# Kernel tuning notes

Hardware: AMD Instinct MI355X
Metric: run time of the kernel (lower is better)

## Reference

```python
import jax, jax.numpy as jnp
import numpy as np
from jax import lax

KS = 10      # kernel_size (asserted == 10 in the torch module)
DCT_N = 10   # dct_n


def _dct_pair(N):
    k = np.arange(N)[:, None]
    i = np.arange(N)[None, :]
    w = np.full((N, 1), np.sqrt(2.0 / N))
    w[0, 0] = np.sqrt(1.0 / N)
    d = w * np.cos(np.pi * (i + 0.5) * k / N)
    return jnp.asarray(d, jnp.float32), jnp.asarray(np.linalg.inv(d), jnp.float32)


def _conv1d(x, w):
    # x: [B, C, L], w: [O, C, K], VALID conv (bias=False in torch)
    return lax.conv_general_dilated(x, w, (1,), 'VALID',
                                    dimension_numbers=('NCH', 'OIH', 'NCH'))


def _two_conv(x, w1, w2):
    return jax.nn.relu(_conv1d(jax.nn.relu(_conv1d(x, w1)), w2))


def _gconv(x, w, att, b):
    # GraphConvolution: att @ (x @ w) + b ; x: [B, node, f_in]
    return jnp.einsum('nm,bmo->bno', att, jnp.einsum('bmf,fo->bmo', x, w)) + b


def _gcn(x, gc1_w, gc1_att, gc1_b, gcb_w, gcb_att, gcb_b, gc7_w, gc7_att, gc7_b):
    # Standard motion-prediction GCN (eval mode: BN=identity, dropout off)
    y = jnp.tanh(_gconv(x, gc1_w, gc1_att, gc1_b))
    for s in range(gcb_w.shape[0]):  # small fixed num_stage
        h = jnp.tanh(_gconv(y, gcb_w[s, 0], gcb_att[s, 0], gcb_b[s, 0]))
        h = jnp.tanh(_gconv(h, gcb_w[s, 1], gcb_att[s, 1], gcb_b[s, 1]))
        y = y + h
    return _gconv(y, gc7_w, gc7_att, gc7_b) + x


def _ffc(x, wl, wg):
    # RealFFC(dim=3): spectral branch (rFFT over time, 1x1 conv on real/imag,
    # ReLU, irFFT) + local 1x1 branch. x: [B, 3, F/3, T]
    y = jnp.fft.rfft(x, axis=-1)
    yc = jnp.concatenate([y.real, y.imag], axis=1)            # [B, 6, F/3, K]
    yc = jax.nn.relu(jnp.einsum('oc,bcfk->bofk', wg, yc))
    re, im = jnp.split(yc, 2, axis=1)
    spec = jnp.fft.irfft(re + 1j * im, n=x.shape[-1], axis=-1)
    return jnp.einsum('oc,bcft->boft', wl, x) + spec


def _forward(input_seq, wq1, wq2, wk1, wk2,
             gc1_w, gc1_att, gc1_b, gcb_w, gcb_att, gcb_b,
             gc7_w, gc7_att, gc7_b, mlp_w1, mlp_w2, ffc_wl, ffc_wg,
             output_n, input_n):
    seq = input_seq[:, :input_n]
    B, _, F = seq.shape
    blen = KS + output_n                       # DCT block length (30)
    dctm, idctm = _dct_pair(blen)
    key_seq = jnp.swapaxes(seq, 1, 2)[:, :, :input_n - output_n]
    query_seq = jnp.swapaxes(seq, 1, 2)[:, :, -KS:]
    # im2col-style overlapping temporal blocks -> per-block DCT
    nvb = input_n - blen + 1
    idx = np.arange(blen)[None, :] + np.arange(nvb)[:, None]
    blocks = seq[:, idx]                       # [B, nvb, blen, F]
    # matches torch reshape(...,dct_n,-1).transpose(2,3).reshape: feature-major
    dvb = jnp.einsum('dk,bnkf->bnfd', dctm[:DCT_N], blocks).reshape(B, nvb, -1)
    key_feat = _two_conv(key_seq / 1000.0, wk1, wk2)       # [B, D, nvb]
    query_feat = _two_conv(query_seq / 1000.0, wq1, wq2)   # [B, D, 1]
    score = jnp.einsum('bdq,bdk->bqk', query_feat, key_feat) + 1e-15
    attn = score / jnp.sum(score, axis=2, keepdims=True)   # sum-normalized attention
    attended = jnp.einsum('bqk,bkf->bqf', attn, dvb)[:, 0].reshape(B, F, DCT_N)
    # FFC branch: pad with last frame x10, fold F into (3, F//3)
    ffc_in = jnp.concatenate([seq, jnp.repeat(seq[:, -1:], 10, axis=1)], axis=1)
    ffc_in = jnp.swapaxes(ffc_in, 1, 2).reshape(B, 3, F // 3, input_n + 10)
    ffc_out = _ffc(ffc_in, ffc_wl, ffc_wg).reshape(B, F, input_n + 10)[:, :, :DCT_N]
    ffc_out = jnp.swapaxes(ffc_out, 1, 2)      # [B, DCT_N, F]
    # GCN branch: last KS frames + last frame repeated output_n times
    gidx = np.concatenate([np.arange(input_n - KS, input_n),
                           np.full(output_n, input_n - 1)])
    gcn_in = seq[:, gidx]                      # [B, blen, F]
    dct_in = jnp.einsum('dk,bkf->bfd', dctm[:DCT_N], gcn_in)
    gcn_out = _gcn(dct_in, gc1_w, gc1_att, gc1_b, gcb_w, gcb_att, gcb_b,
                   gc7_w, gc7_att, gc7_b)      # [B, F, DCT_N]
    combined = jnp.concatenate([gcn_out, attended], axis=-1)
    recon = jnp.einsum('kd,bfd->bkf', idctm[:, :DCT_N], combined[:, :, :DCT_N])  # [B, blen, F]
    fused = jnp.swapaxes(jnp.concatenate([recon, ffc_out], axis=1), 1, 2)  # [B, F, blen+DCT_N=40]
    h = jax.nn.relu(jnp.einsum('bft,ot->bfo', fused, mlp_w1))  # Linear(40,256), no bias
    out = jnp.einsum('bfo,to->bft', h, mlp_w2)                 # Linear(256,40), no bias
    out = jnp.swapaxes(out, 1, 2)[:, :DCT_N]   # [B, DCT_N, F]
    return out[:, :, None, :]                  # [B, DCT_N, itera=1, F]


def setup_inputs() -> dict:
    key = jax.random.key(0)
    ks = jax.random.split(key, 20)
    B, T, F, D, NS = 1024, 50, 48, 512, 2
    p = lambda k, shp: jax.random.normal(k, shp, dtype=jnp.float32) * 0.05
    return {
        'input_seq': jax.random.normal(ks[0], (B, T, F), dtype=jnp.float32),
        'wq1': p(ks[1], (D, F, 6)), 'wq2': p(ks[2], (D, D, 5)),
        'wk1': p(ks[3], (D, F, 6)), 'wk2': p(ks[4], (D, D, 5)),
        'gc1_w': p(ks[5], (10, D)), 'gc1_att': p(ks[6], (F, F)), 'gc1_b': p(ks[7], (D,)),
        'gcb_w': p(ks[8], (NS, 2, D, D)), 'gcb_att': p(ks[9], (NS, 2, F, F)),
        'gcb_b': p(ks[10], (NS, 2, D)),
        'gc7_w': p(ks[11], (D, 10)), 'gc7_att': p(ks[12], (F, F)), 'gc7_b': p(ks[13], (10,)),
        'mlp_w1': p(ks[14], (256, 40)), 'mlp_w2': p(ks[15], (40, 256)),
        'ffc_wl': p(ks[16], (3, 3)), 'ffc_wg': p(ks[17], (6, 6)),
        'output_n': 20, 'input_n': 50, 'itera': 1,
    }


def reference(input_seq, wq1, wq2, wk1, wk2, gc1_w, gc1_att, gc1_b,
              gcb_w, gcb_att, gcb_b, gc7_w, gc7_att, gc7_b,
              mlp_w1, mlp_w2, ffc_wl, ffc_wg, output_n, input_n, itera):
    assert itera == 1  # single-iteration path (the torch itera>1 branch is skipped)
    return _forward(input_seq, wq1, wq2, wk1, wk2,
                    gc1_w, gc1_att, gc1_b, gcb_w, gcb_att, gcb_b,
                    gc7_w, gc7_att, gc7_b, mlp_w1, mlp_w2, ffc_wl, ffc_wg,
                    output_n, input_n)
```

## Files before the change

### kernel.cpp

```cpp
#include <hip/hip_runtime.h>
#include <math.h>

#define BB 1024
#define TT 50
#define FF 48
#define EXTN 60
#define NFREQ 31

typedef _Float16 h8 __attribute__((ext_vector_type(8)));
typedef _Float16 h4 __attribute__((ext_vector_type(4)));
typedef float f4 __attribute__((ext_vector_type(4)));

__device__ __forceinline__ float fast_tanh(float x) {
    float e = __expf(2.0f * x);
    return 1.0f - 2.0f * __builtin_amdgcn_rcpf(e + 1.0f);
}

__global__ void prep_kernel(const float* __restrict__ gcb_w, _Float16* __restrict__ P,
                            const float* __restrict__ gc1_w, _Float16* __restrict__ P1,
                            const float* __restrict__ gc7_w, _Float16* __restrict__ P7,
                            const float* __restrict__ mlp_w1, _Float16* __restrict__ Pw1,
                            const float* __restrict__ mlp_w2, _Float16* __restrict__ Pw2,
                            const float* __restrict__ gc1_att, const float* __restrict__ gcb_att,
                            const float* __restrict__ gc7_att, _Float16* __restrict__ attp,
                            _Float16* __restrict__ Pc_hi, _Float16* __restrict__ Pc_lo,
                            _Float16* __restrict__ Pi_hi, _Float16* __restrict__ Pi_lo,
                            float* __restrict__ dctm, float* __restrict__ dtail) {
    int blk = blockIdx.x, tid = threadIdx.x;
    const _Float16 HZ = (_Float16)0.0f;
    if (blk < 512) {
        int z = blk >> 7;
        int idx = ((blk & 127) << 8) | tid;
        int lane = idx & 63, t8 = idx >> 6;
        int nt = t8 & 7, kw = t8 >> 3;
        int ks = kw & 15, wv = kw >> 4;
        int n = wv * 128 + nt * 16 + (lane & 15);
        int k0 = ks * 32 + (lane >> 4) * 8;
        const float* src = gcb_w + (size_t)z * 262144 + n;
        h8 v;
        #pragma unroll
        for (int j = 0; j < 8; ++j) v[j] = (_Float16)src[(size_t)(k0 + j) * 512];
        *(h8*)(P + (size_t)z * 262144 + (size_t)idx * 8) = v;
    } else if (blk < 528) {
        int idx = ((blk - 512) << 8) | tid;
        int lane = idx & 63, t8 = idx >> 6;
        int nt = t8 & 7, kw = t8 >> 3;
        int ks = kw & 1, wv = kw >> 1;
        int n = wv * 128 + nt * 16 + (lane & 15);
        int k0 = ks * 32 + (lane >> 4) * 8;
        h8 v;
        #pragma unroll
        for (int j = 0; j < 8; ++j) v[j] = (k0 + j < 10) ? (_Float16)gc1_w[(k0 + j) * 512 + n] : HZ;
        *(h8*)(P1 + (size_t)idx * 8) = v;
    } else if (blk < 532) {
        int idx = ((blk - 528) << 8) | tid;
        int lane = idx & 63, t8 = idx >> 6;
        int ks = t8 & 3, wv = t8 >> 2;
        int n = lane & 15;
        int k0 = wv * 128 + ks * 32 + (lane >> 4) * 8;
        h8 v;
        #pragma unroll
        for (int j = 0; j < 8; ++j) v[j] = (n < 10) ? (_Float16)gc7_w[(k0 + j) * 10 + n] : HZ;
        *(h8*)(P7 + (size_t)idx * 8) = v;
    } else if (blk < 540) {
        int idx = ((blk - 532) << 8) | tid;
        int lane = idx & 63, t8 = idx >> 6;
        int ks = t8 & 1, q = t8 >> 1;
        int nt = q & 3, wv = q >> 2;
        int o = wv * 64 + nt * 16 + (lane & 15);
        int k0 = ks * 32 + (lane >> 4) * 8;
        h8 v;
        #pragma unroll
        for (int j = 0; j < 8; ++j) v[j] = (k0 + j < 40) ? (_Float16)mlp_w1[o * 40 + k0 + j] : HZ;
        *(h8*)(Pw1 + (size_t)idx * 8) = v;
    } else if (blk < 542) {
        int idx = ((blk - 540) << 8) | tid;
        int lane = idx & 63, ks = idx >> 6;
        int m = lane & 15;
        int k0 = ks * 32 + (lane >> 4) * 8;
        h8 v;
        #pragma unroll
        for (int j = 0; j < 8; ++j) v[j] = (m < 10) ? (_Float16)mlp_w2[m * 256 + k0 + j] : HZ;
        *(h8*)(Pw2 + (size_t)idx * 8) = v;
    } else if (blk < 614) {
        int idx = (blk - 542) * 256 + tid;
        if (idx < 18432) {
            int l = idx / 3072, r = (idx % 3072) / 64, m = idx & 63;
            float v = 0.f;
            if (m < 48) {
                v = (l == 0) ? gc1_att[r * 48 + m]
                  : (l <= 4) ? gcb_att[(l - 1) * 2304 + r * 48 + m]
                             : gc7_att[r * 48 + m];
            }
            attp[idx] = (_Float16)v;
        }
    } else if (blk < 646) {
        int g = (blk - 614) * 256 + tid;
        int tab = g >> 12, e = g & 4095;
        int j = e & 7, lane = (e >> 3) & 63, t8 = e >> 9;
        int ks = t8 & 1, nt = t8 >> 1;
        int n = nt * 16 + (lane & 15);
        int t = ks * 32 + (lane >> 4) * 8 + j;
        double v = 0.0;
        if (t < 60 && n < 62)
            v = (n < 31) ? cos(M_PI * (double)(n * t) / 30.0)
                         : -sin(M_PI * (double)((n - 31) * t) / 30.0);
        _Float16 hi = (_Float16)(float)v;
        if (tab == 0) Pc_hi[e] = hi;
        else          Pc_lo[e] = (_Float16)(float)(v - (double)(float)hi);
    } else if (blk < 654) {
        int g = (blk - 646) * 256 + tid;
        int tab = g >> 10, e = g & 1023;
        int j = e & 7, lane = (e >> 3) & 63, ks = e >> 9;
        int t = lane & 15;
        int kp = ks * 32 + (lane >> 4) * 8 + j;
        double v = 0.0;
        if (kp == 0) v = 1.0 / 60.0;
        else if (kp < 30) v = (2.0 / 60.0) * cos(M_PI * (double)(kp * t) / 30.0);
        else if (kp == 30) v = ((t & 1) ? -1.0 : 1.0) / 60.0;
        else if (kp >= 32 && kp < 61) v = -(2.0 / 60.0) * sin(M_PI * (double)((kp - 31) * t) / 30.0);
        _Float16 hi = (_Float16)(float)v;
        if (tab == 0) Pi_hi[e] = hi;
        else          Pi_lo[e] = (_Float16)(float)(v - (double)(float)hi);
    } else {
        int idx = (blk - 654) * 256 + tid;
        if (idx < 900) {
            int d = idx / 30, k = idx % 30;
            double w = (d == 0) ? sqrt(1.0 / 30.0) : sqrt(2.0 / 30.0);
            dctm[idx] = (float)(w * cos(M_PI * (k + 0.5) * d / 30.0));
        } else if (idx < 910) {
            int d = idx - 900;
            double w = (d == 0) ? sqrt(1.0 / 30.0) : sqrt(2.0 / 30.0);
            double s = 0.0;
            for (int k = 10; k < 30; ++k) s += w * cos(M_PI * (k + 0.5) * d / 30.0);
            dtail[d] = (float)s;
        }
    }
}

template<int KSTEPS, int MODE>
__device__ __forceinline__ void gcn_layer(char* S, char* T,
        const _Float16* __restrict__ Pw, const _Float16* __restrict__ attp,
        const float* __restrict__ bias, h4* sv,
        int lane, int wv, int l16, int quad) {
    h8 ab[3][2];
    #pragma unroll
    for (int it = 0; it < 3; ++it)
        #pragma unroll
        for (int ks = 0; ks < 2; ++ks)
            ab[it][ks] = *(const h8*)(attp + (it * 16 + l16) * 64 + ks * 32 + quad * 8);

    f4 acc[3][8];
    #pragma unroll
    for (int mt = 0; mt < 3; ++mt)
        #pragma unroll
        for (int nt = 0; nt < 8; ++nt) acc[mt][nt] = (f4)0.0f;

    const _Float16* Pb = Pw + (size_t)wv * (KSTEPS * 8 * 512) + lane * 8;
    const int xm = l16 & 7;
    __syncthreads();

    #pragma unroll 2
    for (int ks = 0; ks < KSTEPS; ++ks) {
        h8 a[3], bfr[8];
        #pragma unroll
        for (int nt = 0; nt < 8; ++nt)
            bfr[nt] = *(const h8*)(Pb + (ks * 8 + nt) * 512);
        #pragma unroll
        for (int mt = 0; mt < 3; ++mt)
            a[mt] = *(h8*)(S + (mt * 16 + l16) * 1024 + (((ks * 4 + quad) ^ xm) << 4));
        #pragma unroll
        for (int mt = 0; mt < 3; ++mt)
            #pragma unroll
            for (int nt = 0; nt < 8; ++nt)
                acc[mt][nt] = __builtin_amdgcn_mfma_f32_16x16x32_f16(a[mt], bfr[nt], acc[mt][nt], 0, 0, 0);
    }
    __syncthreads();

    #pragma unroll
    for (int mt = 0; mt < 3; ++mt) {
        h4 hv;
        #pragma unroll
        for (int j = 0; j < 4; ++j) hv[j] = (_Float16)acc[mt][0][j];
        *(h4*)(T + l16 * 144 + (mt * 16 + quad * 4) * 2) = hv;
    }
    asm volatile("s_waitcnt lgkmcnt(0)" ::: "memory");
    h8 tf0 = *(h8*)(T + l16 * 144 + quad * 16);
    h8 tf1 = *(h8*)(T + l16 * 144 + 64 + quad * 16);

    #pragma unroll
    for (int nt = 0; nt < 8; ++nt) {
        char* Tn = T + ((nt + 1) & 1) * 2304;
        if (nt < 7) {
            #pragma unroll
            for (int mt = 0; mt < 3; ++mt) {
                h4 hv;
                #pragma unroll
                for (int j = 0; j < 4; ++j) hv[j] = (_Float16)acc[mt][nt + 1][j];
                *(h4*)(Tn + l16 * 144 + (mt * 16 + quad * 4) * 2) = hv;
            }
        }
        f4 acc2[3];
        #pragma unroll
        for (int it = 0; it < 3; ++it) {
            acc2[it] = __builtin_amdgcn_mfma_f32_16x16x32_f16(tf0, ab[it][0], (f4)0.0f, 0, 0, 0);
            acc2[it] = __builtin_amdgcn_mfma_f32_16x16x32_f16(tf1, ab[it][1], acc2[it], 0, 0, 0);
        }
        if (nt < 7) {
            asm volatile("s_waitcnt lgkmcnt(0)" ::: "memory");
            tf0 = *(h8*)(Tn + l16 * 144 + quad * 16);
            tf1 = *(h8*)(Tn + l16 * 144 + 64 + quad * 16);
        }
        const int c0 = wv * 128 + nt * 16 + quad * 4;
        const f4 bv = *(const f4*)(bias + c0);
        #pragma unroll
        for (int it = 0; it < 3; ++it) {
            int f = it * 16 + l16;
            char* sp = S + f * 1024 + (((c0 >> 3) ^ (f & 7)) << 4) + ((c0 & 7) << 1);
            if (MODE == 1) sv[nt * 3 + it] = *(h4*)sp;
            h4 o;
            #pragma unroll
            for (int j = 0; j < 4; ++j) {
                float v = fast_tanh(acc2[it][j] + bv[j]);
                if (MODE == 2) v += (float)sv[nt * 3 + it][j];
                o[j] = (_Float16)v;
            }
            *(h4*)sp = o;
        }
    }
}

__launch_bounds__(256, 2)
__global__ void gcn_fused_kernel(const float* __restrict__ seq,
                                 const _Float16* __restrict__ P1,
                                 const _Float16* __restrict__ Pm,
                                 const _Float16* __restrict__ P7,
                                 const _Float16* __restrict__ attp,
                                 const float* __restrict__ gc1_b,
                                 const float* __restrict__ gcb_b,
                                 const float* __restrict__ gc7_b,
                                 const float* __restrict__ dctm,
                                 const float* __restrict__ dtail,
                                 _Float16* __restrict__ fush) {
    __shared__ __align__(16) char smem[69888];
    char* S    = smem;
    char* R    = smem + 49152;
    char* dctf = smem + 67584;
    const int tid = threadIdx.x, lane = tid & 63, wv = tid >> 6;
    const int l16 = lane & 15, quad = lane >> 4;
    const int b = blockIdx.x;
    char* T = R + wv * 4608;

    if (tid < 120) *(f4*)(R + tid * 16) = *(const f4*)(seq + (size_t)b * 2400 + 1920 + tid * 4);
    for (int v = tid; v < 310; v += 256)
        ((float*)(R + 2048))[v] = (v < 300) ? dctm[v] : dtail[v - 300];
    __syncthreads();
    for (int v = tid; v < 480; v += 256) {
        int f = v / 10, d = v % 10;
        const float* q = (const float*)R;
        const float* L = (const float*)(R + 2048);
        float a = L[300 + d] * q[9 * 48 + f];
        #pragma unroll
        for (int k = 0; k < 10; ++k) a += L[d * 30 + k] * q[k * 48 + f];
        ((float*)dctf)[f * 12 + d] = a;
    }
    __syncthreads();
    for (int v = tid; v < 384; v += 256) {
        int m = v >> 3, g = v & 7;
        h8 w = (h8)(_Float16)0.0f;
        if (g < 2) {
            #pragma unroll
            for (int j = 0; j < 8; ++j) {
                int d = g * 8 + j;
                if (d < 10) w[j] = (_Float16)((float*)dctf)[m * 12 + d];
            }
        }
        *(h8*)(S + m * 1024 + ((g ^ (m & 7)) << 4)) = w;
    }
    for (int v = tid; v < 384; v += 256) {
        int s = v % 3, rr = v / 3;
        int r = rr & 15, wb = rr >> 4;
        *(h8*)(R + wb * 2304 + r * 144 + 96 + s * 16) = (h8)(_Float16)0.0f;
    }

    h4 sv[24];
    gcn_layer<2, 0>(S, T, P1,          attp,          gc1_b,        sv, lane, wv, l16, quad);
    gcn_layer<16, 1>(S, T, Pm,          attp + 3072,  gcb_b,        sv, lane, wv, l16, quad);
    gcn_layer<16, 2>(S, T, Pm + 262144, attp + 6144,  gcb_b + 512,  sv, lane, wv, l16, quad);
    gcn_layer<16, 1>(S, T, Pm + 524288, attp + 9216,  gcb_b + 1024, sv, lane, wv, l16, quad);
    gcn_layer<16, 2>(S, T, Pm + 786432, attp + 12288, gcb_b + 1536, sv, lane, wv, l16, quad);

    __syncthreads();
    {
        f4 acc[3];
        #pragma unroll
        for (int mt = 0; mt < 3; ++mt) acc[mt] = (f4)0.0f;
        const _Float16* Pb7 = P7 + wv * 2048 + lane * 8;
        #pragma unroll
        for (int ks = 0; ks < 4; ++ks) {
            h8 bfr = *(const h8*)(Pb7 + ks * 512);
            int kh = wv * 128 + ks * 32;
            #pragma unroll
            for (int mt = 0; mt < 3; ++mt) {
                h8 a = *(h8*)(S + (mt * 16 + l16) * 1024 + ((((kh >> 3) + quad) ^ (l16 & 7)) << 4));
                acc[mt] = __builtin_amdgcn_mfma_f32_16x16x32_f16(a, bfr, acc[mt], 0, 0, 0);
            }
        }
        #pragma unroll
        for (int mt = 0; mt < 3; ++mt)
            *(f4*)(R + wv * 3072 + l16 * 192 + (mt * 16 + quad * 4) * 4) = acc[mt];
    }
    __syncthreads();
    if (wv == 0) {
        h4 tw[3]; int ns[3], ms[3];
        #pragma unroll
        for (int q = 0; q < 3; ++q) {
            int idx = lane * 3 + q;
            int n = idx / 12, m0 = (idx % 12) * 4;
            f4 s = *(f4*)(R + n * 192 + m0 * 4);
            s += *(f4*)(R + 3072 + n * 192 + m0 * 4);
            s += *(f4*)(R + 6144 + n * 192 + m0 * 4);
            s += *(f4*)(R + 9216 + n * 192 + m0 * 4);
            h4 h;
            #pragma unroll
            for (int j = 0; j < 4; ++j) h[j] = (_Float16)s[j];
            tw[q] = h; ns[q] = n; ms[q] = m0;
        }
        asm volatile("s_waitcnt lgkmcnt(0)" ::: "memory");
        #pragma unroll
        for (int q = 0; q < 3; ++q) *(h4*)(R + ns[q] * 144 + ms[q] * 2) = tw[q];
        if (lane < 48) {
            int row = lane / 3, s2 = lane % 3;
            *(h8*)(R + row * 144 + 96 + s2 * 16) = (h8)(_Float16)0.0f;
        }
        asm volatile("s_waitcnt lgkmcnt(0)" ::: "memory");
        h8 tf0 = *(h8*)(R + l16 * 144 + quad * 16);
        h8 tf1 = *(h8*)(R + l16 * 144 + 64 + quad * 16);
        const _Float16* a7 = attp + 15360;
        f4 acc2[3];
        #pragma unroll
        for (int it = 0; it < 3; ++it) {
            h8 ab0 = *(const h8*)(a7 + (it * 16 + l16) * 64 + quad * 8);
            h8 ab1 = *(const h8*)(a7 + (it * 16 + l16) * 64 + 32 + quad * 8);
            acc2[it] = __builtin_amdgcn_mfma_f32_16x16x32_f16(tf0, ab0, (f4)0.0f, 0, 0, 0);
            acc2[it] = __builtin_amdgcn_mfma_f32_16x16x32_f16(tf1, ab1, acc2[it], 0, 0, 0);
        }
        char* G = R + 4096;
        #pragma unroll
        for (int it = 0; it < 3; ++it) {
            int f = it * 16 + l16;
            #pragma unroll
            for (int j = 0; j < 4; ++j) {
                int c = quad * 4 + j;
                if (c < 10) {
                    float v = acc2[it][j] + gc7_b[c] + ((float*)dctf)[f * 12 + c];
                    *(float*)(G + f * 64 + c * 4) = v;
                }
            }
        }
    }
    __syncthreads();
    {
        char* G = R + 4096;
        _Float16* fb = fush + (size_t)b * 3456;
        for (int v = tid; v < 1440; v += 256) {
            int f = v / 30, t = v % 30;
            float s = 0.f;
            #pragma unroll
            for (int d = 0; d < 10; ++d) s += dctm[d * 30 + t] * *(float*)(G + f * 64 + d * 4);
            fb[f * 72 + t] = (_Float16)s;
        }
        for (int v = tid; v < 1152; v += 256) {
            int f = v / 24, t = 40 + v % 24;
            fb[f * 72 + t] = (_Float16)0.0f;
        }
    }
}

__launch_bounds__(256, 3)
__global__ void ffc_mlp_kernel(const float* __restrict__ seq,
                               const _Float16* __restrict__ fush,
                               const float* __restrict__ wl,
                               const float* __restrict__ wg,
                               const _Float16* __restrict__ Pw1,
                               const _Float16* __restrict__ Pw2,
                               const _Float16* __restrict__ Pc_hi,
                               const _Float16* __restrict__ Pc_lo,
                               const _Float16* __restrict__ Pi_hi,
                               const _Float16* __restrict__ Pi_lo,
                               float* __restrict__ out) {
    __shared__ __align__(16) char smem[44736];
    float* ext     = (float*)smem;
    char*  extT_hi = smem + 11520;
    char*  extT_lo = smem + 18432;
    char*  Ya_hi   = extT_hi;
    char*  Ya_lo   = extT_lo;
    float* Xre     = (float*)(smem + 25344);
    float* Xim     = (float*)(smem + 31488);
    _Float16* fus  = (_Float16*)(smem + 37632);
    float* wls     = (float*)(smem + 44544);
    float* wgs     = (float*)(smem + 44580);
    _Float16* hlds = (_Float16*)smem;
    char*  R2      = smem + 25344;

    const int b = blockIdx.x, tid = threadIdx.x;
    const int lane = tid & 63, wv = tid >> 6;
    const int l16 = lane & 15, quad = lane >> 4;
    const float* s = seq + (size_t)b * TT * FF;

    for (int idx = tid; idx < EXTN * FF; idx += 256) {
        int t = idx / FF, f = idx % FF;
        ext[idx] = s[(t < TT ? t : TT - 1) * FF + f];
    }
    for (int idx = tid; idx < 64 * FF; idx += 256) {
        int t = idx / FF, f = idx % FF;
        float v = (t < EXTN) ? s[(t < TT ? t : TT - 1) * FF + f] : 0.f;
        _Float16 hi = (_Float16)v;
        ((_Float16*)(extT_hi + f * 144))[t] = hi;
        ((_Float16*)(extT_lo + f * 144))[t] = (_Float16)(v - (float)hi);
    }
    if (tid < 9) wls[tid] = wl[tid];
    if (tid >= 64 && tid < 100) wgs[tid - 64] = wg[tid - 64];
    __syncthreads();

    {
        const int nt = wv;
        f4 acc[3];
        #pragma unroll
        for (int mt = 0; mt < 3; ++mt) acc[mt] = (f4)0.0f;
        #pragma unroll
        for (int ks = 0; ks < 2; ++ks) {
            h8 bhi = *(const h8*)(Pc_hi + (nt * 2 + ks) * 512 + lane * 8);
            h8 blo = *(const h8*)(Pc_lo + (nt * 2 + ks) * 512 + lane * 8);
            #pragma unroll
            for (int mt = 0; mt < 3; ++mt) {
                h8 ahi = *(h8*)(extT_hi + (mt * 16 + l16) * 144 + ks * 64 + quad * 16);
                h8 alo = *(h8*)(extT_lo + (mt * 16 + l16) * 144 + ks * 64 + quad * 16);
                acc[mt] = __builtin_amdgcn_mfma_f32_16x16x32_f16(ahi, bhi, acc[mt], 0, 0, 0);
                acc[mt] = __builtin_amdgcn_mfma_f32_16x16x32_f16(alo, bhi, acc[mt], 0, 0, 0);
                acc[mt] = __builtin_amdgcn_mfma_f32_16x16x32_f16(ahi, blo, acc[mt], 0, 0, 0);
            }
        }
        int n = nt * 16 + l16;
        #pragma unroll
        for (int mt = 0; mt < 3; ++mt)
            #pragma unroll
            for (int i = 0; i < 4; ++i) {
                int f = mt * 16 + quad * 4 + i;
                if (n < 31) Xre[f * 32 + n] = acc[mt][i];
                else if (n < 62) Xim[f * 32 + n - 31] = acc[mt][i];
            }
    }
    for (int v = tid; v < 384; v += 256) {
        int f = v >> 3, g = v & 7;
        *(h8*)((char*)fus + f * 144 + g * 16) =
            *(const h8*)(fush + (size_t)b * 3456 + f * 72 + g * 8);
    }
    __syncthreads();

    for (int idx = tid; idx < 2976; idx += 256) {
        int k = idx % 31; int g = (idx / 31) % 16; int o = idx / (31 * 16);
        float v = wgs[o * 6 + 0] * Xre[g * 32 + k]        + wgs[o * 6 + 1] * Xre[(16 + g) * 32 + k]
                + wgs[o * 6 + 2] * Xre[(32 + g) * 32 + k] + wgs[o * 6 + 3] * Xim[g * 32 + k]
                + wgs[o * 6 + 4] * Xim[(16 + g) * 32 + k] + wgs[o * 6 + 5] * Xim[(32 + g) * 32 + k];
        v = fmaxf(v, 0.f);
        int fr = (o < 3) ? o * 16 + g : (o - 3) * 16 + g;
        int kp = (o < 3) ? k : 31 + k;
        _Float16 hi = (_Float16)v;
        ((_Float16*)(Ya_hi + fr * 144))[kp] = hi;
        ((_Float16*)(Ya_lo + fr * 144))[kp] = (_Float16)(v - (float)hi);
    }
    if (tid < 96) {
        int f = tid >> 1, c = 62 + (tid & 1);
        ((_Float16*)(Ya_hi + f * 144))[c] = (_Float16)0.0f;
        ((_Float16*)(Ya_lo + f * 144))[c] = (_Float16)0.0f;
    }
    __syncthreads();

    if (wv < 3) {
        const int mt = wv;
        f4 ac = (f4)0.0f;
        #pragma unroll
        for (int ks = 0; ks < 2; ++ks) {
            h8 bhi = *(const h8*)(Pi_hi + ks * 512 + lane * 8);
            h8 blo = *(const h8*)(Pi_lo + ks * 512 + lane * 8);
            h8 ahi = *(h8*)(Ya_hi + (mt * 16 + l16) * 144 + ks * 64 + quad * 16);
            h8 alo = *(h8*)(Ya_lo + (mt * 16 + l16) * 144 + ks * 64 + quad * 16);
            ac = __builtin_amdgcn_mfma_f32_16x16x32_f16(ahi, bhi, ac, 0, 0, 0);
            ac = __builtin_amdgcn_mfma_f32_16x16x32_f16(alo, bhi, ac, 0, 0, 0);
            ac = __builtin_amdgcn_mfma_f32_16x16x32_f16(ahi, blo, ac, 0, 0, 0);
        }
        int t = l16;
        if (t < 10) {
            #pragma unroll
            for (int i = 0; i < 4; ++i) {
                int g = quad * 4 + i;
                int f = mt * 16 + g;
                float loc = wls[mt * 3 + 0] * ext[t * FF + g]
                          + wls[mt * 3 + 1] * ext[t * FF + 16 + g]
                          + wls[mt * 3 + 2] * ext[t * FF + 32 + g];
                fus[f * 72 + 30 + t] = (_Float16)(ac[i] + loc);
            }
        }
    }
    __syncthreads();

    f4 acc1[3][4];
    #pragma unroll
    for (int mt = 0; mt < 3; ++mt)
        #pragma unroll
        for (int nt = 0; nt < 4; ++nt) acc1[mt][nt] = (f4)0.0f;
    #pragma unroll
    for (int ks = 0; ks < 2; ++ks) {
        h8 af[3], bf[4];
        #pragma unroll
        for (int mt = 0; mt < 3; ++mt)
            af[mt] = *(h8*)((char*)fus + (mt * 16 + l16) * 144 + ks * 64 + quad * 16);
        #pragma unroll
        for (int nt = 0; nt < 4; ++nt)
            bf[nt] = *(const h8*)(Pw1 + (size_t)(((wv * 4 + nt) * 2 + ks) * 512) + lane * 8);
        #pragma unroll
        for (int mt = 0; mt < 3; ++mt)
            #pragma unroll
            for (int nt = 0; nt < 4; ++nt)
                acc1[mt][nt] = __builtin_amdgcn_mfma_f32_16x16x32_f16(af[mt], bf[nt], acc1[mt][nt], 0, 0, 0);
    }
    __syncthreads();
    #pragma unroll
    for (int mt = 0; mt < 3; ++mt)
        #pragma unroll
        for (int nt = 0; nt < 4; ++nt) {
            int o = wv * 64 + nt * 16 + l16;
            #pragma unroll
            for (int j = 0; j < 4; ++j) {
                int f = mt * 16 + quad * 4 + j;
                hlds[f * 264 + o] = (_Float16)fmaxf(acc1[mt][nt][j], 0.f);
            }
        }
    __syncthreads();
    f4 acc2[3];
    #pragma unroll
    for (int nt3 = 0; nt3 < 3; ++nt3) acc2[nt3] = (f4)0.0f;
    #pragma unroll
    for (int ss = 0; ss < 2; ++ss) {
        int ks = wv * 2 + ss;
        h8 aw = *(const h8*)(Pw2 + (size_t)ks * 512 + lane * 8);
        #pragma unroll
        for (int nt3 = 0; nt3 < 3; ++nt3) {
            h8 bh = *(h8*)((char*)hlds + (nt3 * 16 + l16) * 528 + ks * 64 + quad * 16);
            acc2[nt3] = __builtin_amdgcn_mfma_f32_16x16x32_f16(aw, bh, acc2[nt3], 0, 0, 0);
        }
    }
    #pragma unroll
    for (int nt3 = 0; nt3 < 3; ++nt3)
        *(f4*)(R2 + wv * 3072 + (nt3 * 16 + l16) * 64 + quad * 16) = acc2[nt3];
    __syncthreads();
    for (int v = tid; v < 768; v += 256) {
        int f = v >> 4, t = v & 15;
        float sm = 0.f;
        #pragma unroll
        for (int w4 = 0; w4 < 4; ++w4) sm += *(float*)(R2 + w4 * 3072 + f * 64 + t * 4);
        if (t < 10) out[(size_t)b * 480 + t * 48 + f] = sm;
    }
}

extern "C" void kernel_launch(void* const* d_in, const int* in_sizes, int n_in,
                              void* d_out, int out_size, void* d_ws, size_t ws_size,
                              hipStream_t stream) {
    (void)in_sizes; (void)n_in; (void)out_size;
    const float* seq     = (const float*)d_in[0];
    const float* gc1_w   = (const float*)d_in[5];
    const float* gc1_att = (const float*)d_in[6];
    const float* gc1_b   = (const float*)d_in[7];
    const float* gcb_w   = (const float*)d_in[8];
    const float* gcb_att = (const float*)d_in[9];
    const float* gcb_b   = (const float*)d_in[10];
    const float* gc7_w   = (const float*)d_in[11];
    const float* gc7_att = (const float*)d_in[12];
    const float* gc7_b   = (const float*)d_in[13];
    const float* mlp_w1  = (const float*)d_in[14];
    const float* mlp_w2  = (const float*)d_in[15];
    const float* ffc_wl  = (const float*)d_in[16];
    const float* ffc_wg  = (const float*)d_in[17];
    float* out = (float*)d_out;
    char* ws = (char*)d_ws;

    float*    dctm  = (float*)ws;
    float*    dtail = dctm + 900;
    char*     p0    = ws + 4096;
    _Float16* Pm    = (_Float16*)p0;   p0 += 4 * 262144 * 2;
    _Float16* P1    = (_Float16*)p0;   p0 += 32768 * 2;
    _Float16* P7    = (_Float16*)p0;   p0 += 8192 * 2;
    _Float16* Pw1   = (_Float16*)p0;   p0 += 16384 * 2;
    _Float16* Pw2   = (_Float16*)p0;   p0 += 4096 * 2;
    _Float16* attp  = (_Float16*)p0;   p0 += 18432 * 2;
    _Float16* Pc_hi = (_Float16*)p0;   p0 += 4096 * 2;
    _Float16* Pc_lo = (_Float16*)p0;   p0 += 4096 * 2;
    _Float16* Pi_hi = (_Float16*)p0;   p0 += 1024 * 2;
    _Float16* Pi_lo = (_Float16*)p0;   p0 += 1024 * 2;
    const size_t fixed_bytes = (size_t)(p0 - ws);

    const size_t per_batch = 6912;
    size_t avail = (ws_size > fixed_bytes) ? (ws_size - fixed_bytes) : 0;
    int nc = 1;
    while ((size_t)(BB / nc) * per_batch > avail && nc < 64) nc *= 2;
    int Bc = BB / nc;
    _Float16* fush = (_Float16*)(ws + fixed_bytes);

    prep_kernel<<<658, 256, 0, stream>>>(gcb_w, Pm, gc1_w, P1, gc7_w, P7,
                                         mlp_w1, Pw1, mlp_w2, Pw2,
                                         gc1_att, gcb_att, gc7_att, attp,
                                         Pc_hi, Pc_lo, Pi_hi, Pi_lo, dctm, dtail);

    for (int ci = 0; ci < nc; ++ci) {
        const float* seqc = seq + (size_t)ci * Bc * TT * FF;
        float* outc = out + (size_t)ci * Bc * 480;
        gcn_fused_kernel<<<Bc, 256, 0, stream>>>(seqc, P1, Pm, P7, attp,
                                                 gc1_b, gcb_b, gc7_b, dctm, dtail, fush);
        ffc_mlp_kernel<<<Bc, 256, 0, stream>>>(seqc, fush, ffc_wl, ffc_wg, Pw1, Pw2,
                                               Pc_hi, Pc_lo, Pi_hi, Pi_lo, outc);
    }
}
```

Before: 272.3 us.

## Process two batch elements per GCN block to halve weight fragment loads

The fused GCN kernel now runs 512-thread blocks that each handle two batch samples. Each of the 8 waves covers a 64-column output slice for both samples, so every weight B-fragment loaded from global memory feeds six MFMA row tiles instead of three. This halves global weight traffic per sample. In exchange, LDS use doubles to about 137 KB per block and occupancy drops to one block per CU. The odd-batch case is not handled and the chunk loop assumes Bc is even.

```diff
diff --git a/kernel.cpp b/kernel.cpp
--- a/kernel.cpp
+++ b/kernel.cpp
@@ -138,11 +138,46 @@
     }
 }
 
+#define S_STRIDE 49152
+#define RB_OFF   98304
+#define G_OFF    (98304 + 26624)
+#define DF_OFF   135168
+
 template<int KSTEPS, int MODE>
-__device__ __forceinline__ void gcn_layer(char* S, char* T,
+__device__ __forceinline__ void gcn_layer(char* smem, char* T,
         const _Float16* __restrict__ Pw, const _Float16* __restrict__ attp,
         const float* __restrict__ bias, h4* sv,
-        int lane, int wv, int l16, int quad) {
+        int lane, int wv8, int l16, int quad) {
+    f4 acc[6][4];
+    #pragma unroll
+    for (int m = 0; m < 6; ++m)
+        #pragma unroll
+        for (int n = 0; n < 4; ++n) acc[m][n] = (f4)0.0f;
+
+    const _Float16* Pb = Pw + (size_t)(wv8 >> 1) * (KSTEPS * 8 * 512)
+                            + (size_t)(wv8 & 1) * 2048 + lane * 8;
+    const int xm = l16 & 7;
+    __syncthreads();
+
+    #pragma unroll 2
+    for (int ks = 0; ks < KSTEPS; ++ks) {
+        h8 a[6], bfr[4];
+        #pragma unroll
+        for (int nt = 0; nt < 4; ++nt)
+            bfr[nt] = *(const h8*)(Pb + (ks * 8 + nt) * 512);
+        #pragma unroll
+        for (int zz = 0; zz < 2; ++zz)
+            #pragma unroll
+            for (int mt = 0; mt < 3; ++mt)
+                a[zz * 3 + mt] = *(h8*)(smem + zz * S_STRIDE + (mt * 16 + l16) * 1024
+                                        + (((ks * 4 + quad) ^ xm) << 4));
+        #pragma unroll
+        for (int m = 0; m < 6; ++m)
+            #pragma unroll
+            for (int nt = 0; nt < 4; ++nt)
+                acc[m][nt] = __builtin_amdgcn_mfma_f32_16x16x32_f16(a[m], bfr[nt], acc[m][nt], 0, 0, 0);
+    }
+
     h8 ab[3][2];
     #pragma unroll
     for (int it = 0; it < 3; ++it)
@@ -150,31 +185,6 @@
         for (int ks = 0; ks < 2; ++ks)
             ab[it][ks] = *(const h8*)(attp + (it * 16 + l16) * 64 + ks * 32 + quad * 8);
 
-    f4 acc[3][8];
-    #pragma unroll
-    for (int mt = 0; mt < 3; ++mt)
-        #pragma unroll
-        for (int nt = 0; nt < 8; ++nt) acc[mt][nt] = (f4)0.0f;
-
-    const _Float16* Pb = Pw + (size_t)wv * (KSTEPS * 8 * 512) + lane * 8;
-    const int xm = l16 & 7;
-    __syncthreads();
-
-    #pragma unroll 2
-    for (int ks = 0; ks < KSTEPS; ++ks) {
-        h8 a[3], bfr[8];
-        #pragma unroll
-        for (int nt = 0; nt < 8; ++nt)
-            bfr[nt] = *(const h8*)(Pb + (ks * 8 + nt) * 512);
-        #pragma unroll
-        for (int mt = 0; mt < 3; ++mt)
-            a[mt] = *(h8*)(S + (mt * 16 + l16) * 1024 + (((ks * 4 + quad) ^ xm) << 4));
-        #pragma unroll
-        for (int mt = 0; mt < 3; ++mt)
-            #pragma unroll
-            for (int nt = 0; nt < 8; ++nt)
-                acc[mt][nt] = __builtin_amdgcn_mfma_f32_16x16x32_f16(a[mt], bfr[nt], acc[mt][nt], 0, 0, 0);
-    }
     __syncthreads();
 
     #pragma unroll
@@ -189,14 +199,15 @@
     h8 tf1 = *(h8*)(T + l16 * 144 + 64 + quad * 16);
 
     #pragma unroll
-    for (int nt = 0; nt < 8; ++nt) {
-        char* Tn = T + ((nt + 1) & 1) * 2304;
-        if (nt < 7) {
+    for (int e = 0; e < 8; ++e) {
+        char* Tn = T + ((e + 1) & 1) * 2304;
+        if (e < 7) {
+            int zn = (e + 1) >> 2, nn = (e + 1) & 3;
             #pragma unroll
             for (int mt = 0; mt < 3; ++mt) {
                 h4 hv;
                 #pragma unroll
-                for (int j = 0; j < 4; ++j) hv[j] = (_Float16)acc[mt][nt + 1][j];
+                for (int j = 0; j < 4; ++j) hv[j] = (_Float16)acc[zn * 3 + mt][nn][j];
                 *(h4*)(Tn + l16 * 144 + (mt * 16 + quad * 4) * 2) = hv;
             }
         }
@@ -206,23 +217,24 @@
             acc2[it] = __builtin_amdgcn_mfma_f32_16x16x32_f16(tf0, ab[it][0], (f4)0.0f, 0, 0, 0);
             acc2[it] = __builtin_amdgcn_mfma_f32_16x16x32_f16(tf1, ab[it][1], acc2[it], 0, 0, 0);
         }
-        if (nt < 7) {
+        if (e < 7) {
             asm volatile("s_waitcnt lgkmcnt(0)" ::: "memory");
             tf0 = *(h8*)(Tn + l16 * 144 + quad * 16);
             tf1 = *(h8*)(Tn + l16 * 144 + 64 + quad * 16);
         }
-        const int c0 = wv * 128 + nt * 16 + quad * 4;
+        const int z = e >> 2, nt = e & 3;
+        const int c0 = wv8 * 64 + nt * 16 + quad * 4;
         const f4 bv = *(const f4*)(bias + c0);
         #pragma unroll
         for (int it = 0; it < 3; ++it) {
             int f = it * 16 + l16;
-            char* sp = S + f * 1024 + (((c0 >> 3) ^ (f & 7)) << 4) + ((c0 & 7) << 1);
-            if (MODE == 1) sv[nt * 3 + it] = *(h4*)sp;
+            char* sp = smem + z * S_STRIDE + f * 1024 + (((c0 >> 3) ^ (f & 7)) << 4) + ((c0 & 7) << 1);
+            if (MODE == 1) sv[e * 3 + it] = *(h4*)sp;
             h4 o;
             #pragma unroll
             for (int j = 0; j < 4; ++j) {
                 float v = fast_tanh(acc2[it][j] + bv[j]);
-                if (MODE == 2) v += (float)sv[nt * 3 + it][j];
+                if (MODE == 2) v += (float)sv[e * 3 + it][j];
                 o[j] = (_Float16)v;
             }
             *(h4*)sp = o;
@@ -230,7 +242,7 @@
     }
 }
 
-__launch_bounds__(256, 2)
+__launch_bounds__(512, 1)
 __global__ void gcn_fused_kernel(const float* __restrict__ seq,
                                  const _Float16* __restrict__ P1,
                                  const _Float16* __restrict__ Pm,
@@ -242,85 +254,93 @@
                                  const float* __restrict__ dctm,
                                  const float* __restrict__ dtail,
                                  _Float16* __restrict__ fush) {
-    __shared__ __align__(16) char smem[69888];
-    char* S    = smem;
-    char* R    = smem + 49152;
-    char* dctf = smem + 67584;
-    const int tid = threadIdx.x, lane = tid & 63, wv = tid >> 6;
+    __shared__ __align__(16) char smem[139776];
+    const int tid = threadIdx.x, lane = tid & 63, wv8 = tid >> 6;
     const int l16 = lane & 15, quad = lane >> 4;
-    const int b = blockIdx.x;
-    char* T = R + wv * 4608;
-
-    if (tid < 120) *(f4*)(R + tid * 16) = *(const f4*)(seq + (size_t)b * 2400 + 1920 + tid * 4);
-    for (int v = tid; v < 310; v += 256)
-        ((float*)(R + 2048))[v] = (v < 300) ? dctm[v] : dtail[v - 300];
-    __syncthreads();
-    for (int v = tid; v < 480; v += 256) {
-        int f = v / 10, d = v % 10;
-        const float* q = (const float*)R;
-        const float* L = (const float*)(R + 2048);
-        float a = L[300 + d] * q[9 * 48 + f];
-        #pragma unroll
-        for (int k = 0; k < 10; ++k) a += L[d * 30 + k] * q[k * 48 + f];
-        ((float*)dctf)[f * 12 + d] = a;
-    }
-    __syncthreads();
-    for (int v = tid; v < 384; v += 256) {
-        int m = v >> 3, g = v & 7;
-        h8 w = (h8)(_Float16)0.0f;
-        if (g < 2) {
-            #pragma unroll
-            for (int j = 0; j < 8; ++j) {
-                int d = g * 8 + j;
-                if (d < 10) w[j] = (_Float16)((float*)dctf)[m * 12 + d];
-            }
-        }
-        *(h8*)(S + m * 1024 + ((g ^ (m & 7)) << 4)) = w;
-    }
-    for (int v = tid; v < 384; v += 256) {
-        int s = v % 3, rr = v / 3;
-        int r = rr & 15, wb = rr >> 4;
-        *(h8*)(R + wb * 2304 + r * 144 + 96 + s * 16) = (h8)(_Float16)0.0f;
+    const int z = tid >> 8, ltid = tid & 255;
+    const int b0 = blockIdx.x * 2;
+    char* T = smem + RB_OFF + wv8 * 4608;
+
+    {
+        char* Rz = smem + RB_OFF + z * 4096;
+        char* dctfz = smem + DF_OFF + z * 2304;
+        const float* seqb = seq + (size_t)(b0 + z) * 2400;
+        if (ltid < 120) *(f4*)(Rz + ltid * 16) = *(const f4*)(seqb + 1920 + ltid * 4);
+        for (int v = ltid; v < 310; v += 256)
+            ((float*)(Rz + 2048))[v] = (v < 300) ? dctm[v] : dtail[v - 300];
+        __syncthreads();
+        for (int v = ltid; v < 480; v += 256) {
+            int f = v / 10, d = v % 10;
+            const float* q = (const float*)Rz;
+            const float* L = (const float*)(Rz + 2048);
+            float a = L[300 + d] * q[9 * 48 + f];
+            #pragma unroll
+            for (int k = 0; k < 10; ++k) a += L[d * 30 + k] * q[k * 48 + f];
+            ((float*)dctfz)[f * 12 + d] = a;
+        }
+        __syncthreads();
+        for (int v = ltid; v < 384; v += 256) {
+            int m = v >> 3, g = v & 7;
+            h8 w = (h8)(_Float16)0.0f;
+            if (g < 2) {
+                #pragma unroll
+                for (int j = 0; j < 8; ++j) {
+                    int d = g * 8 + j;
+                    if (d < 10) w[j] = (_Float16)((float*)dctfz)[m * 12 + d];
+                }
+            }
+            *(h8*)(smem + z * S_STRIDE + m * 1024 + ((g ^ (m & 7)) << 4)) = w;
+        }
+        for (int v = tid; v < 768; v += 512) {
+            int s = v % 3, rr = v / 3;
+            int r = rr & 15, wb = rr >> 4;
+            *(h8*)(smem + RB_OFF + wb * 2304 + r * 144 + 96 + s * 16) = (h8)(_Float16)0.0f;
+        }
     }
 
     h4 sv[24];
-    gcn_layer<2, 0>(S, T, P1,          attp,          gc1_b,        sv, lane, wv, l16, quad);
-    gcn_layer<16, 1>(S, T, Pm,          attp + 3072,  gcb_b,        sv, lane, wv, l16, quad);
-    gcn_layer<16, 2>(S, T, Pm + 262144, attp + 6144,  gcb_b + 512,  sv, lane, wv, l16, quad);
-    gcn_layer<16, 1>(S, T, Pm + 524288, attp + 9216,  gcb_b + 1024, sv, lane, wv, l16, quad);
-    gcn_layer<16, 2>(S, T, Pm + 786432, attp + 12288, gcb_b + 1536, sv, lane, wv, l16, quad);
+    gcn_layer<2, 0>(smem, T, P1,          attp,          gc1_b,        sv, lane, wv8, l16, quad);
+    gcn_layer<16, 1>(smem, T, Pm,          attp + 3072,  gcb_b,        sv, lane, wv8, l16, quad);
+    gcn_layer<16, 2>(smem, T, Pm + 262144, attp + 6144,  gcb_b + 512,  sv, lane, wv8, l16, quad);
+    gcn_layer<16, 1>(smem, T, Pm + 524288, attp + 9216,  gcb_b + 1024, sv, lane, wv8, l16, quad);
+    gcn_layer<16, 2>(smem, T, Pm + 786432, attp + 12288, gcb_b + 1536, sv, lane, wv8, l16, quad);
 
     __syncthreads();
     {
+        const int z6 = wv8 >> 2, wvl = wv8 & 3;
+        char* Sz = smem + z6 * S_STRIDE;
         f4 acc[3];
         #pragma unroll
         for (int mt = 0; mt < 3; ++mt) acc[mt] = (f4)0.0f;
-        const _Float16* Pb7 = P7 + wv * 2048 + lane * 8;
+        const _Float16* Pb7 = P7 + wvl * 2048 + lane * 8;
         #pragma unroll
         for (int ks = 0; ks < 4; ++ks) {
             h8 bfr = *(const h8*)(Pb7 + ks * 512);
-            int kh = wv * 128 + ks * 32;
+            int kh = wvl * 128 + ks * 32;
             #pragma unroll
             for (int mt = 0; mt < 3; ++mt) {
-                h8 a = *(h8*)(S + (mt * 16 + l16) * 1024 + ((((kh >> 3) + quad) ^ (l16 & 7)) << 4));
+                h8 a = *(h8*)(Sz + (mt * 16 + l16) * 1024 + ((((kh >> 3) + quad) ^ (l16 & 7)) << 4));
                 acc[mt] = __builtin_amdgcn_mfma_f32_16x16x32_f16(a, bfr, acc[mt], 0, 0, 0);
             }
         }
         #pragma unroll
         for (int mt = 0; mt < 3; ++mt)
-            *(f4*)(R + wv * 3072 + l16 * 192 + (mt * 16 + quad * 4) * 4) = acc[mt];
-    }
-    __syncthreads();
-    if (wv == 0) {
+            *(f4*)(smem + RB_OFF + z6 * 12288 + wvl * 3072 + l16 * 192 + (mt * 16 + quad * 4) * 4) = acc[mt];
+    }
+    __syncthreads();
+    if ((wv8 & 3) == 0) {
+        const int z6 = wv8 >> 2;
+        char* PZ = smem + RB_OFF + z6 * 12288;
+        char* dctfz = smem + DF_OFF + z6 * 2304;
         h4 tw[3]; int ns[3], ms[3];
         #pragma unroll
         for (int q = 0; q < 3; ++q) {
             int idx = lane * 3 + q;
             int n = idx / 12, m0 = (idx % 12) * 4;
-            f4 s = *(f4*)(R + n * 192 + m0 * 4);
-            s += *(f4*)(R + 3072 + n * 192 + m0 * 4);
-            s += *(f4*)(R + 6144 + n * 192 + m0 * 4);
-            s += *(f4*)(R + 9216 + n * 192 + m0 * 4);
+            f4 s = *(f4*)(PZ + n * 192 + m0 * 4);
+            s += *(f4*)(PZ + 3072 + n * 192 + m0 * 4);
+            s += *(f4*)(PZ + 6144 + n * 192 + m0 * 4);
+            s += *(f4*)(PZ + 9216 + n * 192 + m0 * 4);
             h4 h;
             #pragma unroll
             for (int j = 0; j < 4; ++j) h[j] = (_Float16)s[j];
@@ -328,14 +348,14 @@
         }
         asm volatile("s_waitcnt lgkmcnt(0)" ::: "memory");
         #pragma unroll
-        for (int q = 0; q < 3; ++q) *(h4*)(R + ns[q] * 144 + ms[q] * 2) = tw[q];
+        for (int q = 0; q < 3; ++q) *(h4*)(PZ + ns[q] * 144 + ms[q] * 2) = tw[q];
         if (lane < 48) {
             int row = lane / 3, s2 = lane % 3;
-            *(h8*)(R + row * 144 + 96 + s2 * 16) = (h8)(_Float16)0.0f;
+            *(h8*)(PZ + row * 144 + 96 + s2 * 16) = (h8)(_Float16)0.0f;
         }
         asm volatile("s_waitcnt lgkmcnt(0)" ::: "memory");
-        h8 tf0 = *(h8*)(R + l16 * 144 + quad * 16);
-        h8 tf1 = *(h8*)(R + l16 * 144 + 64 + quad * 16);
+        h8 tf0 = *(h8*)(PZ + l16 * 144 + quad * 16);
+        h8 tf1 = *(h8*)(PZ + l16 * 144 + 64 + quad * 16);
         const _Float16* a7 = attp + 15360;
         f4 acc2[3];
         #pragma unroll
@@ -345,7 +365,7 @@
             acc2[it] = __builtin_amdgcn_mfma_f32_16x16x32_f16(tf0, ab0, (f4)0.0f, 0, 0, 0);
             acc2[it] = __builtin_amdgcn_mfma_f32_16x16x32_f16(tf1, ab1, acc2[it], 0, 0, 0);
         }
-        char* G = R + 4096;
+        char* G = smem + G_OFF + z6 * 3072;
         #pragma unroll
         for (int it = 0; it < 3; ++it) {
             int f = it * 16 + l16;
@@ -353,7 +373,7 @@
             for (int j = 0; j < 4; ++j) {
                 int c = quad * 4 + j;
                 if (c < 10) {
-                    float v = acc2[it][j] + gc7_b[c] + ((float*)dctf)[f * 12 + c];
+                    float v = acc2[it][j] + gc7_b[c] + ((float*)dctfz)[f * 12 + c];
                     *(float*)(G + f * 64 + c * 4) = v;
                 }
             }
@@ -361,16 +381,16 @@
     }
     __syncthreads();
     {
-        char* G = R + 4096;
-        _Float16* fb = fush + (size_t)b * 3456;
-        for (int v = tid; v < 1440; v += 256) {
+        char* G = smem + G_OFF + z * 3072;
+        _Float16* fb = fush + (size_t)(b0 + z) * 3456;
+        for (int v = ltid; v < 1440; v += 256) {
             int f = v / 30, t = v % 30;
             float s = 0.f;
             #pragma unroll
             for (int d = 0; d < 10; ++d) s += dctm[d * 30 + t] * *(float*)(G + f * 64 + d * 4);
             fb[f * 72 + t] = (_Float16)s;
         }
-        for (int v = tid; v < 1152; v += 256) {
+        for (int v = ltid; v < 1152; v += 256) {
             int f = v / 24, t = 40 + v % 24;
             fb[f * 72 + t] = (_Float16)0.0f;
         }
@@ -615,8 +635,8 @@
     for (int ci = 0; ci < nc; ++ci) {
         const float* seqc = seq + (size_t)ci * Bc * TT * FF;
         float* outc = out + (size_t)ci * Bc * 480;
-        gcn_fused_kernel<<<Bc, 256, 0, stream>>>(seqc, P1, Pm, P7, attp,
-                                                 gc1_b, gcb_b, gc7_b, dctm, dtail, fush);
+        gcn_fused_kernel<<<Bc / 2, 512, 0, stream>>>(seqc, P1, Pm, P7, attp,
+                                                     gc1_b, gcb_b, gc7_b, dctm, dtail, fush);
         ffc_mlp_kernel<<<Bc, 256, 0, stream>>>(seqc, fush, ffc_wl, ffc_wg, Pw1, Pw2,
                                                Pc_hi, Pc_lo, Pi_hi, Pi_lo, outc);
     }
```

After: 267.2 us. Within noise of the previous version (-1.8%).
